# Kernel optimization log

Measured on AMD Instinct MI355X. Metric: run time of the kernel, lower is better.

Reference implementation:

```python
import jax, jax.numpy as jnp
import numpy as np

N, E, G = 20000, 320000, 32


def setup_inputs() -> dict:
    key = jax.random.key(0)
    ks = list(jax.random.split(key, 16))
    def nrm(i, shape, s):
        return jax.random.normal(ks[i], shape, jnp.float32) * s
    inp = {}
    inp['x'] = nrm(0, (N, 768), 1.0)
    inp['edge_index'] = jax.random.randint(ks[1], (2, E), 0, N)
    inp['batch'] = jnp.sort(jax.random.randint(ks[2], (N,), 0, G))
    # xavier-ish scales
    inp['proj_w'] = nrm(3, (768, 768), 0.036); inp['proj_b'] = jnp.zeros((768,), jnp.float32)
    inp['gat1_w'] = nrm(4, (768, 1024), 0.033)
    inp['att1_src'] = nrm(5, (4, 256), 0.06); inp['att1_dst'] = nrm(6, (4, 256), 0.06)
    inp['gat1_b'] = jnp.zeros((1024,), jnp.float32)
    inp['ln1_g'] = jnp.ones((1024,), jnp.float32); inp['ln1_b'] = jnp.zeros((1024,), jnp.float32)
    inp['gat2_w'] = nrm(7, (1024, 1024), 0.031)
    inp['att2_src'] = nrm(8, (4, 256), 0.06); inp['att2_dst'] = nrm(9, (4, 256), 0.06)
    inp['gat2_b'] = jnp.zeros((1024,), jnp.float32)
    inp['ln2_g'] = jnp.ones((1024,), jnp.float32); inp['ln2_b'] = jnp.zeros((1024,), jnp.float32)
    inp['gat3_w'] = nrm(10, (1024, 256), 0.04)
    inp['att3_src'] = nrm(11, (1, 256), 0.08); inp['att3_dst'] = nrm(12, (1, 256), 0.08)
    inp['gat3_b'] = jnp.zeros((256,), jnp.float32)
    inp['ln3_g'] = jnp.ones((256,), jnp.float32); inp['ln3_b'] = jnp.zeros((256,), jnp.float32)
    inp['cls1_w'] = nrm(13, (768, 128), 0.047); inp['cls1_b'] = jnp.zeros((128,), jnp.float32)
    inp['cls2_w'] = nrm(14, (128, 1), 0.12); inp['cls2_b'] = jnp.zeros((1,), jnp.float32)
    return inp


def layer_norm(x, g, b, eps=1e-5):
    mu = x.mean(-1, keepdims=True)
    v = ((x - mu) ** 2).mean(-1, keepdims=True)
    return (x - mu) * jax.lax.rsqrt(v + eps) * g + b


def gat_conv(x, src, dst, W, a_src, a_dst, bias, concat):
    # PyG GATConv (eval mode): linear -> per-head additive attention ->
    # segment softmax over incoming edges of each dst node -> scatter-sum.
    n = x.shape[0]
    H, C = a_src.shape
    h = (x @ W).reshape(n, H, C)                      # [N,H,C]
    e_s = (h * a_src[None]).sum(-1)                   # [N,H]
    e_d = (h * a_dst[None]).sum(-1)                   # [N,H]
    logits = jax.nn.leaky_relu(e_s[src] + e_d[dst], 0.2)   # [Etot,H]
    m = jax.ops.segment_max(logits, dst, num_segments=n)   # self-loops -> no empty segments
    ex = jnp.exp(logits - m[dst])
    den = jax.ops.segment_sum(ex, dst, num_segments=n)
    alpha = ex / (den[dst] + 1e-16)                   # [Etot,H]
    out = jax.ops.segment_sum(h[src] * alpha[:, :, None], dst, num_segments=n)  # [N,H,C]
    out = out.reshape(n, H * C) if concat else out.mean(axis=1)
    return out + bias


def reference(x, edge_index, batch, proj_w, proj_b,
              gat1_w, att1_src, att1_dst, gat1_b, ln1_g, ln1_b,
              gat2_w, att2_src, att2_dst, gat2_b, ln2_g, ln2_b,
              gat3_w, att3_src, att3_dst, gat3_b, ln3_g, ln3_b,
              cls1_w, cls1_b, cls2_w, cls2_b):
    n = x.shape[0]
    loop = jnp.arange(n)
    src = jnp.concatenate([edge_index[0], loop])  # GATConv adds self-loops
    dst = jnp.concatenate([edge_index[1], loop])
    h = jax.nn.elu(x @ proj_w + proj_b)
    x1 = jax.nn.elu(layer_norm(gat_conv(h, src, dst, gat1_w, att1_src, att1_dst, gat1_b, True), ln1_g, ln1_b))
    x2 = jax.nn.elu(layer_norm(gat_conv(x1, src, dst, gat2_w, att2_src, att2_dst, gat2_b, True), ln2_g, ln2_b)) + x1
    x3 = jax.nn.elu(layer_norm(gat_conv(x2, src, dst, gat3_w, att3_src, att3_dst, gat3_b, False), ln3_g, ln3_b))
    cnt = jax.ops.segment_sum(jnp.ones((n, 1), x3.dtype), batch, num_segments=G)
    s = jax.ops.segment_sum(x3, batch, num_segments=G)
    mean = s / jnp.maximum(cnt, 1.0)
    mx = jax.ops.segment_max(x3, batch, num_segments=G)
    pooled = jnp.concatenate([mean, mx, s], axis=1)   # [G, 3*256]
    out = jax.nn.relu(pooled @ cls1_w + cls1_b) @ cls2_w + cls2_b
    return out.reshape(-1)
```

## Files before the change

### kernel.cpp

```cpp
#include <hip/hip_runtime.h>
#include <math.h>

typedef float floatx4 __attribute__((ext_vector_type(4)));
typedef _Float16 f16x8 __attribute__((ext_vector_type(8)));
typedef _Float16 f16x4 __attribute__((ext_vector_type(4)));

__device__ __forceinline__ unsigned encf(float f) {
    unsigned u = __float_as_uint(f);
    return (u & 0x80000000u) ? ~u : (u | 0x80000000u);
}
__device__ __forceinline__ float decf(unsigned u) {
    u = (u & 0x80000000u) ? (u & 0x7FFFFFFFu) : ~u;
    return __uint_as_float(u);
}
__device__ __forceinline__ void glds16(const void* g, void* l) {
    __builtin_amdgcn_global_load_lds(
        (const __attribute__((address_space(1))) unsigned int*)g,
        (__attribute__((address_space(3))) unsigned int*)l, 16, 0, 0);
}

__global__ __launch_bounds__(256) void cvt_f16_kernel(
    const float* __restrict__ in, _Float16* __restrict__ out, size_t n4)
{
    size_t i = (size_t)blockIdx.x * 256 + threadIdx.x;
    if (i >= n4) return;
    float4 v = ((const float4*)in)[i];
    f16x4 o;
    o[0] = (_Float16)v.x; o[1] = (_Float16)v.y; o[2] = (_Float16)v.z; o[3] = (_Float16)v.w;
    ((f16x4*)out)[i] = o;
}

__global__ __launch_bounds__(256) void wt_kernel(
    const float* __restrict__ w, _Float16* __restrict__ wt, int K, int N)
{
    __shared__ float t[32][33];
    int bx = blockIdx.x * 32, by = blockIdx.y * 32;
    int tx = threadIdx.x & 31, ty = threadIdx.x >> 5;
    for (int r = ty; r < 32; r += 8)
        t[r][tx] = w[(size_t)(by + r) * N + bx + tx];
    __syncthreads();
    for (int r = ty; r < 32; r += 8)
        wt[(size_t)(bx + r) * K + by + tx] = (_Float16)t[tx][r];
}

__global__ __launch_bounds__(256) void gemm_f16(
    const _Float16* __restrict__ A, const _Float16* __restrict__ BT,
    const float* __restrict__ bias, _Float16* __restrict__ C,
    int M, int K, int N, int act)
{
    __shared__ _Float16 Al[128 * 32];
    __shared__ _Float16 Bl[128 * 32];
    int tid = threadIdx.x;
    int lane = tid & 63, wave = tid >> 6;
    int row0 = blockIdx.y * 128, col0 = blockIdx.x * 128;
    int wm = (wave >> 1) * 64, wn = (wave & 1) * 64;
    int l15 = lane & 15, quad = lane >> 4;

    int rg0 = wave * 2, rg1 = rg0 + 1;
    int srow0 = rg0 * 16 + (lane >> 2);
    int srow1 = rg1 * 16 + (lane >> 2);
    int scol = (lane & 3) * 8;
    int arow0 = row0 + srow0; if (arow0 > M - 1) arow0 = M - 1;
    int arow1 = row0 + srow1; if (arow1 > M - 1) arow1 = M - 1;
    const _Float16* gA0 = A + (size_t)arow0 * K + scol;
    const _Float16* gA1 = A + (size_t)arow1 * K + scol;
    const _Float16* gB0 = BT + (size_t)(col0 + srow0) * K + scol;
    const _Float16* gB1 = BT + (size_t)(col0 + srow1) * K + scol;
    _Float16* lA0 = &Al[rg0 * 512];
    _Float16* lA1 = &Al[rg1 * 512];
    _Float16* lB0 = &Bl[rg0 * 512];
    _Float16* lB1 = &Bl[rg1 * 512];

    floatx4 acc[4][4] = {};

    for (int k0 = 0; k0 < K; k0 += 32) {
        glds16(gA0 + k0, lA0);
        glds16(gA1 + k0, lA1);
        glds16(gB0 + k0, lB0);
        glds16(gB1 + k0, lB1);
        __syncthreads();
        f16x8 af[4], bfr[4];
        #pragma unroll
        for (int i = 0; i < 4; i++) {
            af[i]  = *(const f16x8*)&Al[(wm + i * 16 + l15) * 32 + quad * 8];
            bfr[i] = *(const f16x8*)&Bl[(wn + i * 16 + l15) * 32 + quad * 8];
        }
        #pragma unroll
        for (int i = 0; i < 4; i++)
            #pragma unroll
            for (int j = 0; j < 4; j++)
                acc[i][j] = __builtin_amdgcn_mfma_f32_16x16x32_f16(af[i], bfr[j], acc[i][j], 0, 0, 0);
        __syncthreads();
    }

    #pragma unroll
    for (int i = 0; i < 4; i++) {
        #pragma unroll
        for (int v = 0; v < 4; v++) {
            int gr = row0 + wm + i * 16 + quad * 4 + v;
            if (gr >= M) continue;
            #pragma unroll
            for (int j = 0; j < 4; j++) {
                int gc = col0 + wn + j * 16 + l15;
                float val = acc[i][j][v];
                if (bias) val += bias[gc];
                if (act) val = val > 0.f ? val : (expf(val) - 1.f);
                C[(size_t)gr * N + gc] = (_Float16)val;
            }
        }
    }
}

__global__ __launch_bounds__(256) void attn_scores_kernel(
    const _Float16* __restrict__ h, const float* __restrict__ asrc, const float* __restrict__ adst,
    float* __restrict__ es, float* __restrict__ ed, int Nn, int H)
{
    int wid = (blockIdx.x * 256 + threadIdx.x) >> 6;
    int lane = threadIdx.x & 63;
    if (wid >= Nn * H) return;
    int node = wid / H, hh = wid % H;
    const _Float16* hp = h + (size_t)node * H * 256 + hh * 256 + lane * 4;
    f16x4 v = *(const f16x4*)hp;
    float ss = 0.f, sd = 0.f;
    #pragma unroll
    for (int j = 0; j < 4; j++) {
        float f = (float)v[j];
        ss = fmaf(f, asrc[hh * 256 + lane * 4 + j], ss);
        sd = fmaf(f, adst[hh * 256 + lane * 4 + j], sd);
    }
    #pragma unroll
    for (int o = 32; o; o >>= 1) { ss += __shfl_down(ss, o); sd += __shfl_down(sd, o); }
    if (lane == 0) { es[wid] = ss; ed[wid] = sd; }
}

__global__ __launch_bounds__(256) void csr_init(int* __restrict__ deg, int Nn) {
    int i = blockIdx.x * 256 + threadIdx.x;
    if (i < Nn) deg[i] = 1;
}
__global__ __launch_bounds__(256) void csr_count(const int* __restrict__ ei, int* __restrict__ deg, int E) {
    int i = blockIdx.x * 256 + threadIdx.x;
    if (i < E) atomicAdd(&deg[ei[E + i]], 1);
}
__global__ __launch_bounds__(256) void scan1(const int* __restrict__ deg, int* __restrict__ incl,
                                             int* __restrict__ bsums, int Nn) {
    __shared__ int sd[256];
    int idx = blockIdx.x * 256 + threadIdx.x;
    sd[threadIdx.x] = (idx < Nn) ? deg[idx] : 0;
    __syncthreads();
    for (int o = 1; o < 256; o <<= 1) {
        int x = (threadIdx.x >= (unsigned)o) ? sd[threadIdx.x - o] : 0;
        __syncthreads();
        sd[threadIdx.x] += x;
        __syncthreads();
    }
    if (idx < Nn) incl[idx] = sd[threadIdx.x];
    if (threadIdx.x == 255) bsums[blockIdx.x] = sd[255];
}
__global__ void scan2(int* __restrict__ bsums, int nb) {
    if (blockIdx.x == 0 && threadIdx.x == 0) {
        int run = 0;
        for (int i = 0; i < nb; i++) { int v = bsums[i]; bsums[i] = run; run += v; }
    }
}
__global__ __launch_bounds__(256) void scan3(const int* __restrict__ incl, const int* __restrict__ deg,
                                             const int* __restrict__ bsums, int* __restrict__ rowstart,
                                             int* __restrict__ cursor, int Nn) {
    int idx = blockIdx.x * 256 + threadIdx.x;
    if (idx >= Nn) return;
    int rs = incl[idx] - deg[idx] + bsums[blockIdx.x];
    rowstart[idx] = rs;
    cursor[idx] = rs;
}
__global__ __launch_bounds__(256) void csr_fill(const int* __restrict__ ei, int* __restrict__ cursor,
                                                int* __restrict__ csrc, int* __restrict__ cdst,
                                                int E, int Nn) {
    int i = blockIdx.x * 256 + threadIdx.x;
    if (i >= E + Nn) return;
    int s, d;
    if (i < E) { s = ei[i]; d = ei[E + i]; } else { s = d = i - E; }
    int pos = atomicAdd(&cursor[d], 1);
    csrc[pos] = s;
    cdst[pos] = d;
}

template<int H>
__global__ __launch_bounds__(256) void seg_mz(
    const int* __restrict__ rowstart, const int* __restrict__ deg,
    const int* __restrict__ csrc, const float* __restrict__ es,
    const float* __restrict__ ed, float2* __restrict__ mz, int Nn)
{
    int d = (blockIdx.x * 256 + threadIdx.x) >> 6;
    int lane = threadIdx.x & 63;
    if (d >= Nn) return;
    constexpr int S = 64 / H;
    int head = lane & (H - 1);
    int slot = lane / H;
    int st = rowstart[d], dg = deg[d];
    float edv = ed[d * H + head];
    float m = -1e30f;
    for (int j = slot; j < dg; j += S) {
        float l = es[csrc[st + j] * H + head] + edv;
        l = l > 0.f ? l : 0.2f * l;
        m = fmaxf(m, l);
    }
    #pragma unroll
    for (int o = H; o < 64; o <<= 1) m = fmaxf(m, __shfl_xor(m, o));
    float z = 0.f;
    for (int j = slot; j < dg; j += S) {
        float l = es[csrc[st + j] * H + head] + edv;
        l = l > 0.f ? l : 0.2f * l;
        z += expf(l - m);
    }
    #pragma unroll
    for (int o = H; o < 64; o <<= 1) z += __shfl_xor(z, o);
    if (lane < H) mz[d * H + lane] = make_float2(m, 1.f / (z + 1e-16f));
}

template<int H>
__global__ __launch_bounds__(256) void edge_alpha(
    const int* __restrict__ csrc, const int* __restrict__ cdst,
    const float* __restrict__ es, const float* __restrict__ ed,
    const float2* __restrict__ mz, float* __restrict__ wse, int Etot)
{
    int i = blockIdx.x * 256 + threadIdx.x;
    if (i >= Etot) return;
    int s = csrc[i], d = cdst[i];
    float a[H];
    #pragma unroll
    for (int hh = 0; hh < H; hh++) {
        float l = es[s * H + hh] + ed[d * H + hh];
        l = l > 0.f ? l : 0.2f * l;
        float2 mzv = mz[d * H + hh];
        a[hh] = expf(l - mzv.x) * mzv.y;
    }
    #pragma unroll
    for (int hh = 0; hh < H; hh++) wse[(size_t)i * H + hh] = a[hh];
}

template<int H>
__global__ __launch_bounds__(64 * H) void gat_gather(
    const int* __restrict__ rowstart, const int* __restrict__ deg,
    const int* __restrict__ csrc, const float* __restrict__ wse,
    const _Float16* __restrict__ h, _Float16* __restrict__ out)
{
    constexpr int T = 64 * H;
    const int HC = T * 4;
    int d = blockIdx.x;
    int t = threadIdx.x;
    int head2 = t >> 6;
    int st = rowstart[d], dg = deg[d];
    const _Float16* hb = h + (size_t)t * 4;
    float acc0 = 0.f, acc1 = 0.f, acc2 = 0.f, acc3 = 0.f;
    int s = csrc[st];
    float a = wse[(size_t)st * H + head2];
    for (int j = 1; j < dg; j++) {
        int s_n = csrc[st + j];
        float a_n = wse[(size_t)(st + j) * H + head2];
        f16x4 v = *(const f16x4*)(hb + (size_t)s * HC);
        acc0 = fmaf(a, (float)v[0], acc0);
        acc1 = fmaf(a, (float)v[1], acc1);
        acc2 = fmaf(a, (float)v[2], acc2);
        acc3 = fmaf(a, (float)v[3], acc3);
        s = s_n; a = a_n;
    }
    f16x4 v = *(const f16x4*)(hb + (size_t)s * HC);
    acc0 = fmaf(a, (float)v[0], acc0);
    acc1 = fmaf(a, (float)v[1], acc1);
    acc2 = fmaf(a, (float)v[2], acc2);
    acc3 = fmaf(a, (float)v[3], acc3);
    f16x4 o;
    o[0] = (_Float16)acc0; o[1] = (_Float16)acc1; o[2] = (_Float16)acc2; o[3] = (_Float16)acc3;
    *(f16x4*)(out + (size_t)d * HC + t * 4) = o;
}

__global__ __launch_bounds__(256) void ln_elu_kernel(
    const _Float16* __restrict__ agg, const float* __restrict__ bias,
    const float* __restrict__ gam, const float* __restrict__ bet,
    const float* resid, float* out, _Float16* out16, int HC)
{
    int row = blockIdx.x;
    int tid = threadIdx.x;
    int per = HC >> 8;
    float vr[4];
    const _Float16* ap = agg + (size_t)row * HC;
    float sum = 0.f;
    for (int i = 0; i < per; i++) {
        int c = i * 256 + tid;
        float x = (float)ap[c] + bias[c];
        vr[i] = x; sum += x;
    }
    __shared__ float sm[4];
    #pragma unroll
    for (int o = 32; o; o >>= 1) sum += __shfl_down(sum, o);
    if ((tid & 63) == 0) sm[tid >> 6] = sum;
    __syncthreads();
    float mean = (sm[0] + sm[1] + sm[2] + sm[3]) / (float)HC;
    float sq = 0.f;
    for (int i = 0; i < per; i++) { float dd = vr[i] - mean; sq = fmaf(dd, dd, sq); }
    __syncthreads();
    #pragma unroll
    for (int o = 32; o; o >>= 1) sq += __shfl_down(sq, o);
    if ((tid & 63) == 0) sm[tid >> 6] = sq;
    __syncthreads();
    float var = (sm[0] + sm[1] + sm[2] + sm[3]) / (float)HC;
    float rstd = rsqrtf(var + 1e-5f);
    for (int i = 0; i < per; i++) {
        int c = i * 256 + tid;
        float y = (vr[i] - mean) * rstd * gam[c] + bet[c];
        y = y > 0.f ? y : (expf(y) - 1.f);
        if (resid) y += resid[(size_t)row * HC + c];
        out[(size_t)row * HC + c] = y;
        if (out16) out16[(size_t)row * HC + c] = (_Float16)y;
    }
}

__global__ __launch_bounds__(256) void pool_kernel(
    const float* __restrict__ x3, const int* __restrict__ batch,
    float* __restrict__ ps, unsigned* __restrict__ pm, int* __restrict__ cnt, int Nn)
{
    int c = threadIdx.x;
    int n0 = blockIdx.x * 16;
    int end = n0 + 16; if (end > Nn) end = Nn;
    if (n0 >= Nn) return;
    int curg = batch[n0];
    float s = 0.f, m = -1e30f; int k = 0;
    for (int n = n0; n < end; n++) {
        int g = batch[n];
        if (g != curg) {
            atomicAdd(&ps[curg * 256 + c], s);
            atomicMax(&pm[curg * 256 + c], encf(m));
            if (c == 0) atomicAdd(&cnt[curg], k);
            s = 0.f; m = -1e30f; k = 0; curg = g;
        }
        float v = x3[(size_t)n * 256 + c];
        s += v; m = fmaxf(m, v); k++;
    }
    atomicAdd(&ps[curg * 256 + c], s);
    atomicMax(&pm[curg * 256 + c], encf(m));
    if (c == 0) atomicAdd(&cnt[curg], k);
}

__global__ __launch_bounds__(128) void classifier_kernel(
    const float* __restrict__ ps, const unsigned* __restrict__ pm, const int* __restrict__ cnt,
    const float* __restrict__ w1, const float* __restrict__ b1,
    const float* __restrict__ w2, const float* __restrict__ b2, float* __restrict__ out)
{
    int g = blockIdx.x;
    int tid = threadIdx.x;
    __shared__ float pooled[768];
    __shared__ float red[2];
    float c = (float)cnt[g];
    if (c < 1.f) c = 1.f;
    for (int i = tid; i < 256; i += 128) {
        float s = ps[g * 256 + i];
        pooled[i] = s / c;
        pooled[256 + i] = decf(pm[g * 256 + i]);
        pooled[512 + i] = s;
    }
    __syncthreads();
    float acc = b1[tid];
    for (int k = 0; k < 768; k++) acc = fmaf(pooled[k], w1[k * 128 + tid], acc);
    acc = fmaxf(acc, 0.f);
    float v = acc * w2[tid];
    #pragma unroll
    for (int o = 32; o; o >>= 1) v += __shfl_down(v, o);
    if ((tid & 63) == 0) red[tid >> 6] = v;
    __syncthreads();
    if (tid == 0) out[g] = red[0] + red[1] + b2[0];
}

extern "C" void kernel_launch(void* const* d_in, const int* in_sizes, int n_in,
                              void* d_out, int out_size, void* d_ws, size_t ws_size,
                              hipStream_t stream)
{
    const float* x      = (const float*)d_in[0];
    const int*   ei     = (const int*)d_in[1];
    const int*   batch  = (const int*)d_in[2];
    const float* proj_w = (const float*)d_in[3];
    const float* proj_b = (const float*)d_in[4];
    const float* gat1_w = (const float*)d_in[5];
    const float* att1_s = (const float*)d_in[6];
    const float* att1_d = (const float*)d_in[7];
    const float* gat1_b = (const float*)d_in[8];
    const float* ln1_g  = (const float*)d_in[9];
    const float* ln1_b  = (const float*)d_in[10];
    const float* gat2_w = (const float*)d_in[11];
    const float* att2_s = (const float*)d_in[12];
    const float* att2_d = (const float*)d_in[13];
    const float* gat2_b = (const float*)d_in[14];
    const float* ln2_g  = (const float*)d_in[15];
    const float* ln2_b  = (const float*)d_in[16];
    const float* gat3_w = (const float*)d_in[17];
    const float* att3_s = (const float*)d_in[18];
    const float* att3_d = (const float*)d_in[19];
    const float* gat3_b = (const float*)d_in[20];
    const float* ln3_g  = (const float*)d_in[21];
    const float* ln3_b  = (const float*)d_in[22];
    const float* cls1_w = (const float*)d_in[23];
    const float* cls1_b = (const float*)d_in[24];
    const float* cls2_w = (const float*)d_in[25];
    const float* cls2_b = (const float*)d_in[26];

    int Nn = in_sizes[0] / 768;
    int E  = in_sizes[1] / 2;
    int Gg = out_size;
    int Etot = E + Nn;
    int nb  = (Nn + 255) / 256;

    char* w = (char*)d_ws;
    size_t off = 0;
    auto alloc = [&](size_t bytes) -> char* {
        char* r = w + off;
        off += (bytes + 255) & ~(size_t)255;
        return r;
    };
    size_t NB16 = (size_t)Nn * 1024 * sizeof(_Float16);
    size_t NB32 = (size_t)Nn * 1024 * sizeof(float);
    _Float16* P = (_Float16*)alloc(NB16);
    _Float16* Q = (_Float16*)alloc(NB16);
    _Float16* R = (_Float16*)alloc(NB16);
    float*  X = (float*)alloc(NB32);
    _Float16* projT = (_Float16*)alloc((size_t)768 * 768 * 2);
    _Float16* g1T   = (_Float16*)alloc((size_t)1024 * 768 * 2);
    _Float16* g2T   = (_Float16*)alloc((size_t)1024 * 1024 * 2);
    _Float16* g3T   = (_Float16*)alloc((size_t)256 * 1024 * 2);
    float*    es    = (float*)alloc((size_t)Nn * 4 * 4);
    float*    ed_   = (float*)alloc((size_t)Nn * 4 * 4);
    float2*   mz    = (float2*)alloc((size_t)Nn * 4 * 8);
    int*      deg   = (int*)alloc((size_t)Nn * 4);
    int*      incl  = (int*)alloc((size_t)Nn * 4);
    int*      rowst = (int*)alloc((size_t)Nn * 4);
    int*      curs  = (int*)alloc((size_t)Nn * 4);
    int*      bsums = (int*)alloc((size_t)nb * 4);
    int*      csrc  = (int*)alloc((size_t)Etot * 4);
    int*      cdst  = (int*)alloc((size_t)Etot * 4);
    float*    wse   = (float*)alloc((size_t)Etot * 4 * 4);
    float*    ps    = (float*)alloc((size_t)Gg * 256 * 4);
    unsigned* pm    = (unsigned*)alloc((size_t)Gg * 256 * 4);
    int*      cnt   = (int*)alloc(256);

    dim3 blk(256);

    wt_kernel<<<dim3(768 / 32, 768 / 32), blk, 0, stream>>>(proj_w, projT, 768, 768);
    wt_kernel<<<dim3(1024 / 32, 768 / 32), blk, 0, stream>>>(gat1_w, g1T, 768, 1024);
    wt_kernel<<<dim3(1024 / 32, 1024 / 32), blk, 0, stream>>>(gat2_w, g2T, 1024, 1024);
    wt_kernel<<<dim3(256 / 32, 1024 / 32), blk, 0, stream>>>(gat3_w, g3T, 1024, 256);

    {
        size_t n4 = (size_t)Nn * 768 / 4;
        cvt_f16_kernel<<<dim3((unsigned)((n4 + 255) / 256)), blk, 0, stream>>>(x, P, n4);
    }

    csr_init<<<dim3(nb), blk, 0, stream>>>(deg, Nn);
    csr_count<<<dim3((E + 255) / 256), blk, 0, stream>>>(ei, deg, E);
    scan1<<<dim3(nb), blk, 0, stream>>>(deg, incl, bsums, Nn);
    scan2<<<dim3(1), dim3(64), 0, stream>>>(bsums, nb);
    scan3<<<dim3(nb), blk, 0, stream>>>(incl, deg, bsums, rowst, curs, Nn);
    csr_fill<<<dim3((Etot + 255) / 256), blk, 0, stream>>>(ei, curs, csrc, cdst, E, Nn);

    int mg = (Nn + 127) / 128;

    gemm_f16<<<dim3(768 / 128, mg), blk, 0, stream>>>(P, projT, proj_b, Q, Nn, 768, 768, 1);

    auto run_gat = [&](const _Float16* xin16, const _Float16* WT, const float* as_, const float* ad_,
                       const float* gb, const float* lg, const float* lb, const float* resid,
                       _Float16* hbuf, _Float16* aggbuf, float* xout, _Float16* xout16,
                       int K, int H, int C) {
        int HC = H * C;
        gemm_f16<<<dim3(HC / 128, mg), blk, 0, stream>>>(xin16, WT, nullptr, hbuf, Nn, K, HC, 0);
        int nw = Nn * H;
        attn_scores_kernel<<<dim3((nw + 3) / 4), blk, 0, stream>>>(hbuf, as_, ad_, es, ed_, Nn, H);
        if (H == 4) {
            seg_mz<4><<<dim3((Nn + 3) / 4), blk, 0, stream>>>(rowst, deg, csrc, es, ed_, mz, Nn);
            edge_alpha<4><<<dim3((Etot + 255) / 256), blk, 0, stream>>>(csrc, cdst, es, ed_, mz, wse, Etot);
            gat_gather<4><<<dim3(Nn), dim3(256), 0, stream>>>(rowst, deg, csrc, wse, hbuf, aggbuf);
        } else {
            seg_mz<1><<<dim3((Nn + 3) / 4), blk, 0, stream>>>(rowst, deg, csrc, es, ed_, mz, Nn);
            edge_alpha<1><<<dim3((Etot + 255) / 256), blk, 0, stream>>>(csrc, cdst, es, ed_, mz, wse, Etot);
            gat_gather<1><<<dim3(Nn), dim3(64), 0, stream>>>(rowst, deg, csrc, wse, hbuf, aggbuf);
        }
        ln_elu_kernel<<<dim3(Nn), blk, 0, stream>>>(aggbuf, gb, lg, lb, resid, xout, xout16, HC);
    };

    run_gat(Q, g1T, att1_s, att1_d, gat1_b, ln1_g, ln1_b, nullptr, P, R, X, Q, 768, 4, 256);
    run_gat(Q, g2T, att2_s, att2_d, gat2_b, ln2_g, ln2_b, X, P, R, X, Q, 1024, 4, 256);
    run_gat(Q, g3T, att3_s, att3_d, gat3_b, ln3_g, ln3_b, nullptr, P, R, X, nullptr, 1024, 1, 256);

    hipMemsetAsync(ps, 0, (size_t)Gg * 256 * 4, stream);
    hipMemsetAsync(pm, 0, (size_t)Gg * 256 * 4, stream);
    hipMemsetAsync(cnt, 0, (size_t)Gg * 4, stream);
    pool_kernel<<<dim3((Nn + 15) / 16), blk, 0, stream>>>(X, batch, ps, pm, cnt, Nn);
    classifier_kernel<<<dim3(Gg), dim3(128), 0, stream>>>(ps, pm, cnt, cls1_w, cls1_b, cls2_w, cls2_b, (float*)d_out);
}
```

Measured before the change: 926.8 us.

## Double-buffer GEMM LDS tiles and fuse GAT gather with LayerNorm+ELU

The GEMM now double-buffers its LDS tiles, prefetching the next K-slice while MFMAs run on the current one, and drops one barrier per iteration. The GAT neighbour gather is fused with the bias, LayerNorm, ELU and residual epilogue, so the f16 aggregation buffer no longer makes a round trip through global memory and one launch per layer goes away. The gather loop is unrolled by two edges, and edge_alpha writes its four per-head weights as one float4. The trade-off is twice the LDS per GEMM block and a heavier per-node gather kernel.

```diff
diff --git a/kernel.cpp b/kernel.cpp
--- a/kernel.cpp
+++ b/kernel.cpp
@@ -48,8 +48,8 @@
     const float* __restrict__ bias, _Float16* __restrict__ C,
     int M, int K, int N, int act)
 {
-    __shared__ _Float16 Al[128 * 32];
-    __shared__ _Float16 Bl[128 * 32];
+    __shared__ _Float16 Al[2][128 * 32];
+    __shared__ _Float16 Bl[2][128 * 32];
     int tid = threadIdx.x;
     int lane = tid & 63, wave = tid >> 6;
     int row0 = blockIdx.y * 128, col0 = blockIdx.x * 128;
@@ -66,31 +66,36 @@
     const _Float16* gA1 = A + (size_t)arow1 * K + scol;
     const _Float16* gB0 = BT + (size_t)(col0 + srow0) * K + scol;
     const _Float16* gB1 = BT + (size_t)(col0 + srow1) * K + scol;
-    _Float16* lA0 = &Al[rg0 * 512];
-    _Float16* lA1 = &Al[rg1 * 512];
-    _Float16* lB0 = &Bl[rg0 * 512];
-    _Float16* lB1 = &Bl[rg1 * 512];
 
     floatx4 acc[4][4] = {};
 
-    for (int k0 = 0; k0 < K; k0 += 32) {
-        glds16(gA0 + k0, lA0);
-        glds16(gA1 + k0, lA1);
-        glds16(gB0 + k0, lB0);
-        glds16(gB1 + k0, lB1);
+    glds16(gA0, &Al[0][rg0 * 512]);
+    glds16(gA1, &Al[0][rg1 * 512]);
+    glds16(gB0, &Bl[0][rg0 * 512]);
+    glds16(gB1, &Bl[0][rg1 * 512]);
+
+    int nk = K >> 5;
+    for (int it = 0; it < nk; it++) {
+        int cur = it & 1, nxt = cur ^ 1;
         __syncthreads();
+        if (it + 1 < nk) {
+            int k1 = (it + 1) << 5;
+            glds16(gA0 + k1, &Al[nxt][rg0 * 512]);
+            glds16(gA1 + k1, &Al[nxt][rg1 * 512]);
+            glds16(gB0 + k1, &Bl[nxt][rg0 * 512]);
+            glds16(gB1 + k1, &Bl[nxt][rg1 * 512]);
+        }
         f16x8 af[4], bfr[4];
         #pragma unroll
         for (int i = 0; i < 4; i++) {
-            af[i]  = *(const f16x8*)&Al[(wm + i * 16 + l15) * 32 + quad * 8];
-            bfr[i] = *(const f16x8*)&Bl[(wn + i * 16 + l15) * 32 + quad * 8];
+            af[i]  = *(const f16x8*)&Al[cur][(wm + i * 16 + l15) * 32 + quad * 8];
+            bfr[i] = *(const f16x8*)&Bl[cur][(wn + i * 16 + l15) * 32 + quad * 8];
         }
         #pragma unroll
         for (int i = 0; i < 4; i++)
             #pragma unroll
             for (int j = 0; j < 4; j++)
                 acc[i][j] = __builtin_amdgcn_mfma_f32_16x16x32_f16(af[i], bfr[j], acc[i][j], 0, 0, 0);
-        __syncthreads();
     }
 
     #pragma unroll
@@ -233,84 +238,97 @@
         float2 mzv = mz[d * H + hh];
         a[hh] = expf(l - mzv.x) * mzv.y;
     }
-    #pragma unroll
-    for (int hh = 0; hh < H; hh++) wse[(size_t)i * H + hh] = a[hh];
+    if constexpr (H == 4) {
+        ((float4*)wse)[i] = make_float4(a[0], a[1], a[2], a[3]);
+    } else {
+        wse[i] = a[0];
+    }
 }
 
 template<int H>
-__global__ __launch_bounds__(64 * H) void gat_gather(
+__global__ __launch_bounds__(64 * H) void gat_gather_ln(
     const int* __restrict__ rowstart, const int* __restrict__ deg,
     const int* __restrict__ csrc, const float* __restrict__ wse,
-    const _Float16* __restrict__ h, _Float16* __restrict__ out)
+    const _Float16* __restrict__ h,
+    const float* __restrict__ bias, const float* __restrict__ gam,
+    const float* __restrict__ bet, const float* resid,
+    float* xout, _Float16* xout16)
 {
     constexpr int T = 64 * H;
+    constexpr int NW = H;
     const int HC = T * 4;
     int d = blockIdx.x;
     int t = threadIdx.x;
+    int lane = t & 63, wave = t >> 6;
     int head2 = t >> 6;
     int st = rowstart[d], dg = deg[d];
     const _Float16* hb = h + (size_t)t * 4;
-    float acc0 = 0.f, acc1 = 0.f, acc2 = 0.f, acc3 = 0.f;
-    int s = csrc[st];
-    float a = wse[(size_t)st * H + head2];
-    for (int j = 1; j < dg; j++) {
-        int s_n = csrc[st + j];
-        float a_n = wse[(size_t)(st + j) * H + head2];
-        f16x4 v = *(const f16x4*)(hb + (size_t)s * HC);
-        acc0 = fmaf(a, (float)v[0], acc0);
-        acc1 = fmaf(a, (float)v[1], acc1);
-        acc2 = fmaf(a, (float)v[2], acc2);
-        acc3 = fmaf(a, (float)v[3], acc3);
-        s = s_n; a = a_n;
-    }
-    f16x4 v = *(const f16x4*)(hb + (size_t)s * HC);
-    acc0 = fmaf(a, (float)v[0], acc0);
-    acc1 = fmaf(a, (float)v[1], acc1);
-    acc2 = fmaf(a, (float)v[2], acc2);
-    acc3 = fmaf(a, (float)v[3], acc3);
-    f16x4 o;
-    o[0] = (_Float16)acc0; o[1] = (_Float16)acc1; o[2] = (_Float16)acc2; o[3] = (_Float16)acc3;
-    *(f16x4*)(out + (size_t)d * HC + t * 4) = o;
-}
-
-__global__ __launch_bounds__(256) void ln_elu_kernel(
-    const _Float16* __restrict__ agg, const float* __restrict__ bias,
-    const float* __restrict__ gam, const float* __restrict__ bet,
-    const float* resid, float* out, _Float16* out16, int HC)
-{
-    int row = blockIdx.x;
-    int tid = threadIdx.x;
-    int per = HC >> 8;
-    float vr[4];
-    const _Float16* ap = agg + (size_t)row * HC;
-    float sum = 0.f;
-    for (int i = 0; i < per; i++) {
-        int c = i * 256 + tid;
-        float x = (float)ap[c] + bias[c];
-        vr[i] = x; sum += x;
-    }
-    __shared__ float sm[4];
+
+    float a0 = 0.f, a1 = 0.f, a2 = 0.f, a3 = 0.f;
+    int j = 0;
+    for (; j + 2 <= dg; j += 2) {
+        int s0 = csrc[st + j], s1 = csrc[st + j + 1];
+        float w0 = wse[(size_t)(st + j) * H + head2];
+        float w1 = wse[(size_t)(st + j + 1) * H + head2];
+        f16x4 v0 = *(const f16x4*)(hb + (size_t)s0 * HC);
+        f16x4 v1 = *(const f16x4*)(hb + (size_t)s1 * HC);
+        a0 += w0 * (float)v0[0] + w1 * (float)v1[0];
+        a1 += w0 * (float)v0[1] + w1 * (float)v1[1];
+        a2 += w0 * (float)v0[2] + w1 * (float)v1[2];
+        a3 += w0 * (float)v0[3] + w1 * (float)v1[3];
+    }
+    if (j < dg) {
+        int s0 = csrc[st + j];
+        float w0 = wse[(size_t)(st + j) * H + head2];
+        f16x4 v0 = *(const f16x4*)(hb + (size_t)s0 * HC);
+        a0 += w0 * (float)v0[0];
+        a1 += w0 * (float)v0[1];
+        a2 += w0 * (float)v0[2];
+        a3 += w0 * (float)v0[3];
+    }
+
+    int c0 = t * 4;
+    a0 += bias[c0]; a1 += bias[c0 + 1]; a2 += bias[c0 + 2]; a3 += bias[c0 + 3];
+
+    __shared__ float sm[NW];
+    float sum = a0 + a1 + a2 + a3;
     #pragma unroll
     for (int o = 32; o; o >>= 1) sum += __shfl_down(sum, o);
-    if ((tid & 63) == 0) sm[tid >> 6] = sum;
-    __syncthreads();
-    float mean = (sm[0] + sm[1] + sm[2] + sm[3]) / (float)HC;
-    float sq = 0.f;
-    for (int i = 0; i < per; i++) { float dd = vr[i] - mean; sq = fmaf(dd, dd, sq); }
-    __syncthreads();
+    if (lane == 0) sm[wave] = sum;
+    __syncthreads();
+    float tot = 0.f;
+    #pragma unroll
+    for (int w2 = 0; w2 < NW; w2++) tot += sm[w2];
+    float mean = tot / (float)HC;
+    float d0 = a0 - mean, d1 = a1 - mean, d2 = a2 - mean, d3 = a3 - mean;
+    float sq = d0 * d0 + d1 * d1 + d2 * d2 + d3 * d3;
     #pragma unroll
     for (int o = 32; o; o >>= 1) sq += __shfl_down(sq, o);
-    if ((tid & 63) == 0) sm[tid >> 6] = sq;
-    __syncthreads();
-    float var = (sm[0] + sm[1] + sm[2] + sm[3]) / (float)HC;
-    float rstd = rsqrtf(var + 1e-5f);
-    for (int i = 0; i < per; i++) {
-        int c = i * 256 + tid;
-        float y = (vr[i] - mean) * rstd * gam[c] + bet[c];
-        y = y > 0.f ? y : (expf(y) - 1.f);
-        if (resid) y += resid[(size_t)row * HC + c];
-        out[(size_t)row * HC + c] = y;
-        if (out16) out16[(size_t)row * HC + c] = (_Float16)y;
+    __syncthreads();
+    if (lane == 0) sm[wave] = sq;
+    __syncthreads();
+    tot = 0.f;
+    #pragma unroll
+    for (int w2 = 0; w2 < NW; w2++) tot += sm[w2];
+    float rstd = rsqrtf(tot / (float)HC + 1e-5f);
+
+    float y0 = d0 * rstd * gam[c0]     + bet[c0];
+    float y1 = d1 * rstd * gam[c0 + 1] + bet[c0 + 1];
+    float y2 = d2 * rstd * gam[c0 + 2] + bet[c0 + 2];
+    float y3 = d3 * rstd * gam[c0 + 3] + bet[c0 + 3];
+    y0 = y0 > 0.f ? y0 : (expf(y0) - 1.f);
+    y1 = y1 > 0.f ? y1 : (expf(y1) - 1.f);
+    y2 = y2 > 0.f ? y2 : (expf(y2) - 1.f);
+    y3 = y3 > 0.f ? y3 : (expf(y3) - 1.f);
+    if (resid) {
+        float4 r = ((const float4*)resid)[(size_t)d * T + t];
+        y0 += r.x; y1 += r.y; y2 += r.z; y3 += r.w;
+    }
+    ((float4*)xout)[(size_t)d * T + t] = make_float4(y0, y1, y2, y3);
+    if (xout16) {
+        f16x4 o;
+        o[0] = (_Float16)y0; o[1] = (_Float16)y1; o[2] = (_Float16)y2; o[3] = (_Float16)y3;
+        ((f16x4*)xout16)[(size_t)d * T + t] = o;
     }
 }
 
@@ -418,7 +436,6 @@
     size_t NB32 = (size_t)Nn * 1024 * sizeof(float);
     _Float16* P = (_Float16*)alloc(NB16);
     _Float16* Q = (_Float16*)alloc(NB16);
-    _Float16* R = (_Float16*)alloc(NB16);
     float*  X = (float*)alloc(NB32);
     _Float16* projT = (_Float16*)alloc((size_t)768 * 768 * 2);
     _Float16* g1T   = (_Float16*)alloc((size_t)1024 * 768 * 2);
@@ -464,7 +481,7 @@
 
     auto run_gat = [&](const _Float16* xin16, const _Float16* WT, const float* as_, const float* ad_,
                        const float* gb, const float* lg, const float* lb, const float* resid,
-                       _Float16* hbuf, _Float16* aggbuf, float* xout, _Float16* xout16,
+                       _Float16* hbuf, float* xout, _Float16* xout16,
                        int K, int H, int C) {
         int HC = H * C;
         gemm_f16<<<dim3(HC / 128, mg), blk, 0, stream>>>(xin16, WT, nullptr, hbuf, Nn, K, HC, 0);
@@ -473,18 +490,19 @@
         if (H == 4) {
             seg_mz<4><<<dim3((Nn + 3) / 4), blk, 0, stream>>>(rowst, deg, csrc, es, ed_, mz, Nn);
             edge_alpha<4><<<dim3((Etot + 255) / 256), blk, 0, stream>>>(csrc, cdst, es, ed_, mz, wse, Etot);
-            gat_gather<4><<<dim3(Nn), dim3(256), 0, stream>>>(rowst, deg, csrc, wse, hbuf, aggbuf);
+            gat_gather_ln<4><<<dim3(Nn), dim3(256), 0, stream>>>(rowst, deg, csrc, wse, hbuf,
+                                                                 gb, lg, lb, resid, xout, xout16);
         } else {
             seg_mz<1><<<dim3((Nn + 3) / 4), blk, 0, stream>>>(rowst, deg, csrc, es, ed_, mz, Nn);
             edge_alpha<1><<<dim3((Etot + 255) / 256), blk, 0, stream>>>(csrc, cdst, es, ed_, mz, wse, Etot);
-            gat_gather<1><<<dim3(Nn), dim3(64), 0, stream>>>(rowst, deg, csrc, wse, hbuf, aggbuf);
+            gat_gather_ln<1><<<dim3(Nn), dim3(64), 0, stream>>>(rowst, deg, csrc, wse, hbuf,
+                                                                gb, lg, lb, resid, xout, xout16);
         }
-        ln_elu_kernel<<<dim3(Nn), blk, 0, stream>>>(aggbuf, gb, lg, lb, resid, xout, xout16, HC);
     };
 
-    run_gat(Q, g1T, att1_s, att1_d, gat1_b, ln1_g, ln1_b, nullptr, P, R, X, Q, 768, 4, 256);
-    run_gat(Q, g2T, att2_s, att2_d, gat2_b, ln2_g, ln2_b, X, P, R, X, Q, 1024, 4, 256);
-    run_gat(Q, g3T, att3_s, att3_d, gat3_b, ln3_g, ln3_b, nullptr, P, R, X, nullptr, 1024, 1, 256);
+    run_gat(Q, g1T, att1_s, att1_d, gat1_b, ln1_g, ln1_b, nullptr, P, X, Q, 768, 4, 256);
+    run_gat(Q, g2T, att2_s, att2_d, gat2_b, ln2_g, ln2_b, X, P, X, Q, 1024, 4, 256);
+    run_gat(Q, g3T, att3_s, att3_d, gat3_b, ln3_g, ln3_b, nullptr, P, X, nullptr, 1024, 1, 256);
 
     hipMemsetAsync(ps, 0, (size_t)Gg * 256 * 4, stream);
     hipMemsetAsync(pm, 0, (size_t)Gg * 256 * 4, stream);
```

Result: faster. 814.2 us (-12.1%).
